# Kernel optimization log

Hardware: AMD Instinct MI355X
Metric: run time of the kernel (lower is better)

Reference implementation:

```python
import jax, jax.numpy as jnp
import numpy as np

NUM_USER = 50000
NUM_ITEM = 30000
N = NUM_USER + NUM_ITEM
E = 300000
DIM = 64
NUM_ROUTING = 3
EPS = 1e-12
SLOPE = 0.01  # torch leaky_relu default negative slope


def l2norm(x):
    return x / jnp.sqrt(jnp.sum(x * x, axis=-1, keepdims=True) + EPS)


def gat_conv(x, src, dst):
    # GRCN GATConv: alpha_e = softmax_{e: dst(e)=i}( <x_i, x_j> ), out_i = sum alpha_e * x_j
    xi = x[dst]                      # [E', D]
    xj = x[src]                      # [E', D]
    a = jnp.sum(xi * xj, axis=-1)    # [E']
    m = jax.ops.segment_max(a, dst, num_segments=N)
    m = jnp.where(jnp.isfinite(m), m, 0.0)  # nodes with no incoming edges
    ea = jnp.exp(a - m[dst])
    s = jax.ops.segment_sum(ea, dst, num_segments=N)
    alpha = ea / (s[dst] + EPS)
    out = jax.ops.segment_sum(xj * alpha[:, None], dst, num_segments=N)
    return out, alpha


def sage_conv(x, src, dst, w_e, W, b):
    # GRCN SAGEConv(aggr='add') with edge weights: out = (sum_j w_e * x_j) @ W + b
    agg = jax.ops.segment_sum(x[src] * w_e, dst, num_segments=N)
    return agg @ W + b


def cgcn(feat, Wm, bm, pref, edge_u, edge_i, src2, dst2):
    f = jax.nn.leaky_relu(feat @ Wm + bm, SLOPE)   # MLP projection, [num_item, D]
    pref = l2norm(pref)
    f = l2norm(f)
    for _ in range(NUM_ROUTING):
        x = jnp.concatenate([pref, f], axis=0)     # [N, D]
        xh, _ = gat_conv(x, edge_i, edge_u)        # items -> users only
        pref = l2norm(pref + xh[:NUM_USER])
    x = jnp.concatenate([pref, f], axis=0)
    xh, alpha = gat_conv(x, src2, dst2)            # doubled (bidirectional) edges
    xh = jax.nn.leaky_relu(xh, SLOPE)
    return x + xh, alpha[:, None]                  # [N, D], [2E, 1]


def egcn(id_emb, src2, dst2, w, W1, b1, W2, b2):
    x = l2norm(id_emb)
    x1 = jax.nn.leaky_relu(sage_conv(x, src2, dst2, w, W1, b1), SLOPE)
    x2 = jax.nn.leaky_relu(sage_conv(x1, src2, dst2, w, W2, b2), SLOPE)
    return x + x1 + x2


def setup_inputs() -> dict:
    key = jax.random.key(0)
    ks = jax.random.split(key, 16)
    edge_u = jax.random.randint(ks[0], (E,), 0, NUM_USER)
    edge_i = jax.random.randint(ks[1], (E,), NUM_USER, N)  # items offset by NUM_USER
    xav = lambda k, sh: jax.random.normal(k, sh, jnp.float32) * np.float32(np.sqrt(2.0 / (sh[0] + sh[1])))
    return {
        'edge_u': edge_u,
        'edge_i': edge_i,
        'v_feat': jax.random.normal(ks[2], (NUM_ITEM, 2048), jnp.float32),
        'a_feat': jax.random.normal(ks[3], (NUM_ITEM, 128), jnp.float32),
        'pref_v': xav(ks[4], (NUM_USER, DIM)),
        'pref_a': xav(ks[5], (NUM_USER, DIM)),
        'Wv': xav(ks[6], (2048, DIM)),
        'bv': jnp.zeros((DIM,), jnp.float32),
        'Wa': xav(ks[7], (128, DIM)),
        'ba': jnp.zeros((DIM,), jnp.float32),
        'id_emb': xav(ks[8], (N, DIM)),
        'W1': xav(ks[9], (DIM, DIM)),
        'b1': jnp.zeros((DIM,), jnp.float32),
        'W2': xav(ks[10], (DIM, DIM)),
        'b2': jnp.zeros((DIM,), jnp.float32),
        'conf': xav(ks[11], (N, 2)),
    }


def reference(edge_u, edge_i, v_feat, a_feat, pref_v, pref_a, Wv, bv, Wa, ba,
              id_emb, W1, b1, W2, b2, conf):
    # doubled edge list: edge_index cat edge_index[[1,0]], target = row 0
    src2 = jnp.concatenate([edge_i, edge_u])       # [2E]
    dst2 = jnp.concatenate([edge_u, edge_i])       # [2E]

    v_rep, w_v = cgcn(v_feat, Wv, bv, pref_v, edge_u, edge_i, src2, dst2)
    a_rep, w_a = cgcn(a_feat, Wa, ba, pref_a, edge_u, edge_i, src2, dst2)

    weight = jnp.concatenate([w_v, w_a], axis=1)   # [2E, 2]
    # 'confid' mode: confidence = cat(conf[edge[0]], conf[edge[1]]) == conf[dst2]
    confidence = conf[dst2]                        # [2E, 2]
    weight = jnp.max(weight * confidence, axis=1, keepdims=True)  # [2E, 1]
    weight = jax.nn.relu(weight)                   # pruning

    id_rep = egcn(id_emb, src2, dst2, weight, W1, b1, W2, b2)
    # fusion_mode == 'concat'
    return jnp.concatenate([id_rep, v_rep, a_rep], axis=1)  # [N, 3*DIM]
```

## Files before the change

### kernel.cpp

```cpp
#include <hip/hip_runtime.h>
#include <hip/hip_bf16.h>

#define NU 50000
#define NI 30000
#define NN 80000
#define EE 300000
#define E2 600000
#define EPSF 1e-12f
#define SLOPE_ 0.01f
#define NB_SCAN ((NN + 255)/256)

__device__ __forceinline__ float leaky(float v){ return v>0.f? v : SLOPE_*v; }

__device__ __forceinline__ float qred16(float v){
  v += __shfl_xor(v, 1, 16);
  v += __shfl_xor(v, 2, 16);
  v += __shfl_xor(v, 4, 16);
  v += __shfl_xor(v, 8, 16);
  return v;
}
__device__ __forceinline__ float4 qnorm(float4 v){
  float ss = qred16(v.x*v.x + v.y*v.y + v.z*v.z + v.w*v.w);
  float inv = 1.f/sqrtf(ss + EPSF);
  v.x*=inv; v.y*=inv; v.z*=inv; v.w*=inv;
  return v;
}

typedef __attribute__((address_space(3))) unsigned int lds_u32;
typedef const __attribute__((address_space(1))) unsigned int glb_u32;
__device__ __forceinline__ void gld16(const float* g, float* l){
  __builtin_amdgcn_global_load_lds((glb_u32*)g, (lds_u32*)l, 16, 0, 0);
}

__global__ void k_hist(const int* __restrict__ eu, const int* __restrict__ ei, int* __restrict__ cnt){
  int e = blockIdx.x*blockDim.x + threadIdx.x;
  if(e<EE){ atomicAdd(&cnt[eu[e]],1); atomicAdd(&cnt[ei[e]],1); }
}

__global__ void k_scanA(const int* __restrict__ cnt, int* __restrict__ loc, int* __restrict__ bsum){
  __shared__ int sm[256];
  int t = threadIdx.x;
  int i = blockIdx.x*256 + t;
  int v = (i<NN) ? cnt[i] : 0;
  sm[t] = v; __syncthreads();
  #pragma unroll
  for(int off=1; off<256; off<<=1){
    int u = (t>=off) ? sm[t-off] : 0;
    __syncthreads();
    sm[t] += u;
    __syncthreads();
  }
  if(i<NN) loc[i] = sm[t] - v;
  if(t==255) bsum[blockIdx.x] = sm[255];
}

__global__ void k_scanB(int* __restrict__ bsum, int* __restrict__ boff){
  __shared__ int sm[512];
  int t = threadIdx.x;
  int v = (t<NB_SCAN) ? bsum[t] : 0;
  sm[t] = v; __syncthreads();
  #pragma unroll
  for(int off=1; off<512; off<<=1){
    int u = (t>=off) ? sm[t-off] : 0;
    __syncthreads();
    sm[t] += u;
    __syncthreads();
  }
  if(t<NB_SCAN) boff[t] = sm[t] - v;
}

__global__ void k_scanC(const int* __restrict__ loc, const int* __restrict__ boff,
                        int* __restrict__ ptr, int* __restrict__ cur){
  int i = blockIdx.x*256 + threadIdx.x;
  if(i<NN){
    int p = loc[i] + boff[blockIdx.x];
    ptr[i] = p; cur[i] = p;
  }
  if(i==0) ptr[NN] = E2;
}

__global__ void k_scatter(const int* __restrict__ eu, const int* __restrict__ ei,
                          int* __restrict__ cur, int* __restrict__ colA, int* __restrict__ dstA){
  int e = blockIdx.x*blockDim.x + threadIdx.x;
  if(e<EE){
    int u = eu[e], it = ei[e];
    int s1 = atomicAdd(&cur[u],1);  colA[s1]=it; dstA[s1]=u;
    int s2 = atomicAdd(&cur[it],1); colA[s2]=u;  dstA[s2]=it;
  }
}

__global__ void k_l2n4(const float* __restrict__ in, float* __restrict__ out, int rows){
  int idx = blockIdx.x*blockDim.x + threadIdx.x;
  int g = idx>>4, c = idx&15;
  if(g>=rows) return;
  float4 v = *(const float4*)(in + (size_t)g*64 + 4*c);
  *(float4*)(out + (size_t)g*64 + 4*c) = qnorm(v);
}

template<int K, int KS>
__global__ __launch_bounds__(256,4) void k_pg(const float* __restrict__ feat,
    const float* __restrict__ W, float* __restrict__ part, int rows){
  __shared__ float As[64*64];
  __shared__ float Ws[64*64];
  const int KSL = K/KS;
  const int STEPS = KSL/64;
  int t = threadIdx.x;
  int w = t>>6, lane = t&63;
  int c = t&15, rg = t>>4;
  int rowb = blockIdx.x*64;
  int k0 = blockIdx.y*KSL;
  float4 acc[4];
  #pragma unroll
  for(int r=0;r<4;r++) acc[r] = make_float4(0.f,0.f,0.f,0.f);

  for(int s=0; s<STEPS; ++s){
    if(s) __syncthreads();
    int kk = k0 + s*64;
    #pragma unroll
    for(int i=0;i<4;i++){
      int q = w*4 + i;
      int trow = q*4 + (lane>>4);
      int grow = rowb + trow; if(grow > rows-1) grow = rows-1;
      int seg = (lane&15) ^ (q&3);
      gld16(feat + (size_t)grow*K + kk + seg*4, As + q*256);
    }
    #pragma unroll
    for(int i=0;i<4;i++){
      int q = w*4 + i;
      gld16(W + (size_t)(kk + q*4)*64 + lane*4, Ws + q*256);
    }
    __syncthreads();
    #pragma unroll 4
    for(int k4=0;k4<16;k4++){
      float4 wv[4], a4[4];
      #pragma unroll
      for(int j=0;j<4;j++) wv[j] = *(const float4*)&Ws[(k4*4+j)*64 + c*4];
      int sw = (k4 ^ (rg&3))*4;
      #pragma unroll
      for(int r=0;r<4;r++) a4[r] = *(const float4*)&As[(rg*4+r)*64 + sw];
      #pragma unroll
      for(int r=0;r<4;r++){
        acc[r].x += a4[r].x*wv[0].x + a4[r].y*wv[1].x + a4[r].z*wv[2].x + a4[r].w*wv[3].x;
        acc[r].y += a4[r].x*wv[0].y + a4[r].y*wv[1].y + a4[r].z*wv[2].y + a4[r].w*wv[3].y;
        acc[r].z += a4[r].x*wv[0].z + a4[r].y*wv[1].z + a4[r].z*wv[2].z + a4[r].w*wv[3].z;
        acc[r].w += a4[r].x*wv[0].w + a4[r].y*wv[1].w + a4[r].z*wv[2].w + a4[r].w*wv[3].w;
      }
    }
  }
  float* pb = part + (size_t)blockIdx.y*rows*64;
  #pragma unroll
  for(int r=0;r<4;r++){
    int row = rowb + rg*4 + r;
    if(row < rows) *(float4*)(pb + (size_t)row*64 + c*4) = acc[r];
  }
}

template<int KS>
__global__ void k_projfin(const float* __restrict__ part, const float* __restrict__ bias,
    float* __restrict__ xout, int rows){
  int idx = blockIdx.x*blockDim.x + threadIdx.x;
  int g = idx>>4, c = idx&15;
  if(g>=rows) return;
  float4 o = make_float4(0.f,0.f,0.f,0.f);
  #pragma unroll
  for(int s=0;s<KS;s++){
    float4 p = *(const float4*)(part + ((size_t)s*rows + g)*64 + 4*c);
    o.x += p.x; o.y += p.y; o.z += p.z; o.w += p.w;
  }
  float4 bb = *(const float4*)(bias + 4*c);
  o.x = leaky(o.x + bb.x); o.y = leaky(o.y + bb.y);
  o.z = leaky(o.z + bb.z); o.w = leaky(o.w + bb.w);
  *(float4*)(xout + (size_t)g*128 + 4*c) = qnorm(o);
}

__global__ void k_route3(const float* __restrict__ pv, const float* __restrict__ pa,
    float* __restrict__ xc, const int* __restrict__ ptr, const int* __restrict__ col){
  int g = blockIdx.x*(blockDim.x>>4) + (threadIdx.x>>4);
  int c = threadIdx.x & 15;
  if(g >= NU) return;
  float4 uv = qnorm(*(const float4*)(pv + (size_t)g*64 + 4*c));
  float4 ua = qnorm(*(const float4*)(pa + (size_t)g*64 + 4*c));
  int e0 = ptr[g], e1 = ptr[g+1];
  #pragma unroll 1
  for(int it=0; it<3; ++it){
    float sv = 0.f, sa = 0.f;
    float4 cv = make_float4(0.f,0.f,0.f,0.f);
    float4 ca = make_float4(0.f,0.f,0.f,0.f);
    for(int e=e0; e<e1; e++){
      int src = col[e];
      float4 jv = *(const float4*)(xc + (size_t)src*128 + 4*c);
      float4 ja = *(const float4*)(xc + (size_t)src*128 + 64 + 4*c);
      float dv = qred16(uv.x*jv.x + uv.y*jv.y + uv.z*jv.z + uv.w*jv.w);
      float da = qred16(ua.x*ja.x + ua.y*ja.y + ua.z*ja.z + ua.w*ja.w);
      float ev = __expf(dv), ea = __expf(da);
      sv += ev; sa += ea;
      cv.x += ev*jv.x; cv.y += ev*jv.y; cv.z += ev*jv.z; cv.w += ev*jv.w;
      ca.x += ea*ja.x; ca.y += ea*ja.y; ca.z += ea*ja.z; ca.w += ea*ja.w;
    }
    float iv = 1.f/(sv + EPSF), ia = 1.f/(sa + EPSF);
    uv = qnorm(make_float4(uv.x + cv.x*iv, uv.y + cv.y*iv, uv.z + cv.z*iv, uv.w + cv.w*iv));
    ua = qnorm(make_float4(ua.x + ca.x*ia, ua.y + ca.y*ia, ua.z + ca.z*ia, ua.w + ca.w*ia));
  }
  *(float4*)(xc + (size_t)g*128 + 4*c) = uv;
  *(float4*)(xc + (size_t)g*128 + 64 + 4*c) = ua;
}

__global__ void k_fgat(const float* __restrict__ xc,
    float* __restrict__ av, float* __restrict__ aa,
    float* __restrict__ sv, float* __restrict__ sa,
    const int* __restrict__ ptr, const int* __restrict__ col,
    float* __restrict__ out){
  int g = blockIdx.x*(blockDim.x>>4) + (threadIdx.x>>4);
  int c = threadIdx.x & 15;
  if(g >= NN) return;
  float4 iv = *(const float4*)(xc + (size_t)g*128 + 4*c);
  float4 ia = *(const float4*)(xc + (size_t)g*128 + 64 + 4*c);
  int e0 = ptr[g], e1 = ptr[g+1];
  float smv = 0.f, sma = 0.f;
  float4 cv = make_float4(0.f,0.f,0.f,0.f);
  float4 ca = make_float4(0.f,0.f,0.f,0.f);
  for(int e=e0; e<e1; e++){
    int src = col[e];
    float4 jv = *(const float4*)(xc + (size_t)src*128 + 4*c);
    float4 ja = *(const float4*)(xc + (size_t)src*128 + 64 + 4*c);
    float dv = qred16(iv.x*jv.x + iv.y*jv.y + iv.z*jv.z + iv.w*jv.w);
    float da = qred16(ia.x*ja.x + ia.y*ja.y + ia.z*ja.z + ia.w*ja.w);
    float ev = __expf(dv), ea = __expf(da);
    if(c==0){ av[e] = ev; aa[e] = ea; }
    smv += ev; sma += ea;
    cv.x += ev*jv.x; cv.y += ev*jv.y; cv.z += ev*jv.z; cv.w += ev*jv.w;
    ca.x += ea*ja.x; ca.y += ea*ja.y; ca.z += ea*ja.z; ca.w += ea*ja.w;
  }
  float invv = 1.f/(smv + EPSF), inva = 1.f/(sma + EPSF);
  if(c==0){ sv[g] = invv; sa[g] = inva; }
  float4 ov = make_float4(iv.x + leaky(cv.x*invv), iv.y + leaky(cv.y*invv),
                          iv.z + leaky(cv.z*invv), iv.w + leaky(cv.w*invv));
  float4 oa = make_float4(ia.x + leaky(ca.x*inva), ia.y + leaky(ca.y*inva),
                          ia.z + leaky(ca.z*inva), ia.w + leaky(ca.w*inva));
  *(float4*)(out + (size_t)g*192 + 64  + 4*c) = ov;
  *(float4*)(out + (size_t)g*192 + 128 + 4*c) = oa;
}

__global__ void k_weight(const float* __restrict__ av, const float* __restrict__ aa,
    const float* __restrict__ sv, const float* __restrict__ sa,
    const int* __restrict__ dstA, const float* __restrict__ conf, float* __restrict__ w){
  int e = blockIdx.x*blockDim.x + threadIdx.x;
  if(e >= E2) return;
  int d = dstA[e];
  float wv = av[e]*sv[d]*conf[2*d+0];
  float wa = aa[e]*sa[d]*conf[2*d+1];
  float m = fmaxf(wv, wa);
  w[e] = (m > 0.f) ? m : 0.f;
}

template<int EPI>
__global__ __launch_bounds__(256) void k_aggmm(const float* __restrict__ xin,
    const float* __restrict__ wb, const int* __restrict__ ptr, const int* __restrict__ col,
    const float* __restrict__ Wm, const float* __restrict__ bm,
    const float* __restrict__ a0, const float* __restrict__ a1,
    float* __restrict__ outp){
  __shared__ float Wl[64*64];
  __shared__ float rowbuf[16*68];
  int t = threadIdx.x;
  #pragma unroll
  for(int i=0;i<4;i++)
    *(float4*)&Wl[i*1024 + t*4] = *(const float4*)&Wm[i*1024 + t*4];
  int grp = t>>4, c = t&15;
  int g = blockIdx.x*16 + grp;
  bool ok = g < NN;
  int e0 = ok ? ptr[g] : 0, e1 = ok ? ptr[g+1] : 0;
  float4 acc = make_float4(0.f,0.f,0.f,0.f);
  for(int e=e0; e<e1; e++){
    float we = wb[e];
    float4 xs = *(const float4*)(xin + (size_t)col[e]*64 + 4*c);
    acc.x += we*xs.x; acc.y += we*xs.y; acc.z += we*xs.z; acc.w += we*xs.w;
  }
  __syncthreads();
  *(float4*)&rowbuf[grp*68 + c*4] = acc;
  float4 o = make_float4(0.f,0.f,0.f,0.f);
  #pragma unroll 4
  for(int k4=0;k4<16;k4++){
    float4 a4 = *(const float4*)&rowbuf[grp*68 + k4*4];
    float4 w0 = *(const float4*)&Wl[(k4*4+0)*64 + c*4];
    float4 w1 = *(const float4*)&Wl[(k4*4+1)*64 + c*4];
    float4 w2 = *(const float4*)&Wl[(k4*4+2)*64 + c*4];
    float4 w3 = *(const float4*)&Wl[(k4*4+3)*64 + c*4];
    o.x += a4.x*w0.x + a4.y*w1.x + a4.z*w2.x + a4.w*w3.x;
    o.y += a4.x*w0.y + a4.y*w1.y + a4.z*w2.y + a4.w*w3.y;
    o.z += a4.x*w0.z + a4.y*w1.z + a4.z*w2.z + a4.w*w3.z;
    o.w += a4.x*w0.w + a4.y*w1.w + a4.z*w2.w + a4.w*w3.w;
  }
  if(!ok) return;
  float4 bb = *(const float4*)(bm + 4*c);
  o.x = leaky(o.x + bb.x); o.y = leaky(o.y + bb.y);
  o.z = leaky(o.z + bb.z); o.w = leaky(o.w + bb.w);
  if(EPI==0){
    *(float4*)(outp + (size_t)g*64 + 4*c) = o;
  }else{
    float4 v0 = *(const float4*)(a0 + (size_t)g*64 + 4*c);
    float4 v1 = *(const float4*)(a1 + (size_t)g*64 + 4*c);
    o.x += v0.x + v1.x; o.y += v0.y + v1.y;
    o.z += v0.z + v1.z; o.w += v0.w + v1.w;
    *(float4*)(outp + (size_t)g*192 + 4*c) = o;
  }
}

extern "C" void kernel_launch(void* const* d_in, const int* in_sizes, int n_in,
                              void* d_out, int out_size, void* d_ws, size_t ws_size,
                              hipStream_t stream){
  const int*   edge_u = (const int*)  d_in[0];
  const int*   edge_i = (const int*)  d_in[1];
  const float* v_feat = (const float*)d_in[2];
  const float* a_feat = (const float*)d_in[3];
  const float* pref_v = (const float*)d_in[4];
  const float* pref_a = (const float*)d_in[5];
  const float* Wv     = (const float*)d_in[6];
  const float* bv     = (const float*)d_in[7];
  const float* Wa     = (const float*)d_in[8];
  const float* ba     = (const float*)d_in[9];
  const float* id_emb = (const float*)d_in[10];
  const float* W1     = (const float*)d_in[11];
  const float* b1     = (const float*)d_in[12];
  const float* W2     = (const float*)d_in[13];
  const float* b2     = (const float*)d_in[14];
  const float* conf   = (const float*)d_in[15];
  float* out = (float*)d_out;

  char* p = (char*)d_ws;
  auto alloc = [&](size_t bytes)->void*{
    void* q = p; p += (bytes + 255) & ~(size_t)255; return q;
  };
  int*   cnt  = (int*)  alloc((size_t)NN*4);
  int*   loc  = (int*)  alloc((size_t)NN*4);
  int*   bsum = (int*)  alloc((size_t)NB_SCAN*4);
  int*   boff = (int*)  alloc((size_t)NB_SCAN*4);
  int*   ptr  = (int*)  alloc((size_t)(NN+1)*4);
  int*   cur  = (int*)  alloc((size_t)NN*4);
  int*   colA = (int*)  alloc((size_t)E2*4);
  int*   dstA = (int*)  alloc((size_t)E2*4);
  float* xc   = (float*)alloc((size_t)NN*128*4);
  float* x0   = (float*)alloc((size_t)NN*64*4);
  float* x1   = (float*)alloc((size_t)NN*64*4);
  float* av   = (float*)alloc((size_t)E2*4);
  float* aa   = (float*)alloc((size_t)E2*4);
  float* sv   = (float*)alloc((size_t)NN*4);
  float* sa   = (float*)alloc((size_t)NN*4);
  float* wb   = (float*)alloc((size_t)E2*4);
  float* part = x0;

  hipMemsetAsync(cnt, 0, (size_t)NN*4, stream);
  k_hist<<<(EE+255)/256, 256, 0, stream>>>(edge_u, edge_i, cnt);
  k_scanA<<<NB_SCAN, 256, 0, stream>>>(cnt, loc, bsum);
  k_scanB<<<1, 512, 0, stream>>>(bsum, boff);
  k_scanC<<<NB_SCAN, 256, 0, stream>>>(loc, boff, ptr, cur);
  k_scatter<<<(EE+255)/256, 256, 0, stream>>>(edge_u, edge_i, cur, colA, dstA);

  k_pg<2048,4><<<dim3((NI+63)/64, 4), 256, 0, stream>>>(v_feat, Wv, part, NI);
  k_projfin<4><<<(NI*16+255)/256, 256, 0, stream>>>(part, bv, xc + (size_t)NU*128, NI);
  k_pg<128,2><<<dim3((NI+63)/64, 2), 256, 0, stream>>>(a_feat, Wa, part, NI);
  k_projfin<2><<<(NI*16+255)/256, 256, 0, stream>>>(part, ba, xc + (size_t)NU*128 + 64, NI);

  k_l2n4<<<(NN*16+255)/256, 256, 0, stream>>>(id_emb, x0, NN);

  k_route3<<<(NU+15)/16, 256, 0, stream>>>(pref_v, pref_a, xc, ptr, colA);

  k_fgat<<<(NN+15)/16, 256, 0, stream>>>(xc, av, aa, sv, sa, ptr, colA, out);

  k_weight<<<(E2+255)/256, 256, 0, stream>>>(av, aa, sv, sa, dstA, conf, wb);

  k_aggmm<0><<<(NN+15)/16, 256, 0, stream>>>(x0, wb, ptr, colA, W1, b1, nullptr, nullptr, x1);
  k_aggmm<1><<<(NN+15)/16, 256, 0, stream>>>(x1, wb, ptr, colA, W2, b2, x0, x1, out);
}
```

Before: 751.3 us.

## Fuse edge-weight kernel into aggmm, widen gather groups, enlarge projection tile

Several changes land together. The k_weight kernel and the dstA array are removed, and the pruned edge weights are now computed inside the first aggregation kernel using per-destination sums and confidences. The route and final GAT kernels now use 32-lane groups covering both modalities in one row, with neighbour loops unrolled by two for more memory-level parallelism. The visual projection GEMM moves to a 128-row tile to increase reuse of the weight tile. Together these cut a launch and the dstA traffic and improve gather throughput, at the cost of higher register use in the larger GEMM tile.

```diff
diff --git a/kernel.cpp b/kernel.cpp
--- a/kernel.cpp
+++ b/kernel.cpp
@@ -25,6 +25,9 @@
   v.x*=inv; v.y*=inv; v.z*=inv; v.w*=inv;
   return v;
 }
+__device__ __forceinline__ float dot4(float4 a, float4 b){
+  return a.x*b.x + a.y*b.y + a.z*b.z + a.w*b.w;
+}
 
 typedef __attribute__((address_space(3))) unsigned int lds_u32;
 typedef const __attribute__((address_space(1))) unsigned int glb_u32;
@@ -80,12 +83,12 @@
 }
 
 __global__ void k_scatter(const int* __restrict__ eu, const int* __restrict__ ei,
-                          int* __restrict__ cur, int* __restrict__ colA, int* __restrict__ dstA){
+                          int* __restrict__ cur, int* __restrict__ colA){
   int e = blockIdx.x*blockDim.x + threadIdx.x;
   if(e<EE){
     int u = eu[e], it = ei[e];
-    int s1 = atomicAdd(&cur[u],1);  colA[s1]=it; dstA[s1]=u;
-    int s2 = atomicAdd(&cur[it],1); colA[s2]=u;  dstA[s2]=it;
+    int s1 = atomicAdd(&cur[u],1);  colA[s1]=it;
+    int s2 = atomicAdd(&cur[it],1); colA[s2]=u;
   }
 }
 
@@ -95,6 +98,63 @@
   if(g>=rows) return;
   float4 v = *(const float4*)(in + (size_t)g*64 + 4*c);
   *(float4*)(out + (size_t)g*64 + 4*c) = qnorm(v);
+}
+
+template<int K, int KS>
+__global__ __launch_bounds__(256,4) void k_pg128(const float* __restrict__ feat,
+    const float* __restrict__ W, float* __restrict__ part, int rows){
+  __shared__ float As[128*64];
+  __shared__ float Ws[64*64];
+  const int KSL = K/KS;
+  const int STEPS = KSL/64;
+  int t = threadIdx.x;
+  int w = t>>6, lane = t&63;
+  int c = t&15, rg = t>>4;
+  int rowb = blockIdx.x*128;
+  int k0 = blockIdx.y*KSL;
+  float4 acc[8];
+  #pragma unroll
+  for(int r=0;r<8;r++) acc[r] = make_float4(0.f,0.f,0.f,0.f);
+
+  for(int s=0; s<STEPS; ++s){
+    if(s) __syncthreads();
+    int kk = k0 + s*64;
+    #pragma unroll
+    for(int i=0;i<8;i++){
+      int q = w*8 + i;
+      int grow = rowb + q*4 + (lane>>4); if(grow > rows-1) grow = rows-1;
+      int seg = (lane&15) ^ (q&3);
+      gld16(feat + (size_t)grow*K + kk + seg*4, As + q*256);
+    }
+    #pragma unroll
+    for(int i=0;i<4;i++){
+      int q = w*4 + i;
+      gld16(W + (size_t)(kk + q*4)*64 + lane*4, Ws + q*256);
+    }
+    __syncthreads();
+    #pragma unroll 2
+    for(int k4=0;k4<16;k4++){
+      float4 wv[4];
+      #pragma unroll
+      for(int j=0;j<4;j++) wv[j] = *(const float4*)&Ws[(k4*4+j)*64 + c*4];
+      #pragma unroll
+      for(int r=0;r<8;r++){
+        int row = rg*8 + r;
+        int sw = (k4 ^ ((row>>2)&3))*4;
+        float4 a4 = *(const float4*)&As[row*64 + sw];
+        acc[r].x += a4.x*wv[0].x + a4.y*wv[1].x + a4.z*wv[2].x + a4.w*wv[3].x;
+        acc[r].y += a4.x*wv[0].y + a4.y*wv[1].y + a4.z*wv[2].y + a4.w*wv[3].y;
+        acc[r].z += a4.x*wv[0].z + a4.y*wv[1].z + a4.z*wv[2].z + a4.w*wv[3].z;
+        acc[r].w += a4.x*wv[0].w + a4.y*wv[1].w + a4.z*wv[2].w + a4.w*wv[3].w;
+      }
+    }
+  }
+  float* pb = part + (size_t)blockIdx.y*rows*64;
+  #pragma unroll
+  for(int r=0;r<8;r++){
+    int row = rowb + rg*8 + r;
+    if(row < rows) *(float4*)(pb + (size_t)row*64 + c*4) = acc[r];
+  }
 }
 
 template<int K, int KS>
@@ -119,8 +179,7 @@
     #pragma unroll
     for(int i=0;i<4;i++){
       int q = w*4 + i;
-      int trow = q*4 + (lane>>4);
-      int grow = rowb + trow; if(grow > rows-1) grow = rows-1;
+      int grow = rowb + q*4 + (lane>>4); if(grow > rows-1) grow = rows-1;
       int seg = (lane&15) ^ (q&3);
       gld16(feat + (size_t)grow*K + kk + seg*4, As + q*256);
     }
@@ -175,34 +234,40 @@
 
 __global__ void k_route3(const float* __restrict__ pv, const float* __restrict__ pa,
     float* __restrict__ xc, const int* __restrict__ ptr, const int* __restrict__ col){
-  int g = blockIdx.x*(blockDim.x>>4) + (threadIdx.x>>4);
-  int c = threadIdx.x & 15;
+  int g = blockIdx.x*8 + (threadIdx.x>>5);
+  int c = threadIdx.x & 31;
   if(g >= NU) return;
-  float4 uv = qnorm(*(const float4*)(pv + (size_t)g*64 + 4*c));
-  float4 ua = qnorm(*(const float4*)(pa + (size_t)g*64 + 4*c));
+  float4 u = (c<16) ? *(const float4*)(pv + (size_t)g*64 + 4*c)
+                    : *(const float4*)(pa + (size_t)g*64 + 4*(c-16));
+  u = qnorm(u);
   int e0 = ptr[g], e1 = ptr[g+1];
   #pragma unroll 1
   for(int it=0; it<3; ++it){
-    float sv = 0.f, sa = 0.f;
-    float4 cv = make_float4(0.f,0.f,0.f,0.f);
-    float4 ca = make_float4(0.f,0.f,0.f,0.f);
-    for(int e=e0; e<e1; e++){
-      int src = col[e];
-      float4 jv = *(const float4*)(xc + (size_t)src*128 + 4*c);
-      float4 ja = *(const float4*)(xc + (size_t)src*128 + 64 + 4*c);
-      float dv = qred16(uv.x*jv.x + uv.y*jv.y + uv.z*jv.z + uv.w*jv.w);
-      float da = qred16(ua.x*ja.x + ua.y*ja.y + ua.z*ja.z + ua.w*ja.w);
-      float ev = __expf(dv), ea = __expf(da);
-      sv += ev; sa += ea;
-      cv.x += ev*jv.x; cv.y += ev*jv.y; cv.z += ev*jv.z; cv.w += ev*jv.w;
-      ca.x += ea*ja.x; ca.y += ea*ja.y; ca.z += ea*ja.z; ca.w += ea*ja.w;
-    }
-    float iv = 1.f/(sv + EPSF), ia = 1.f/(sa + EPSF);
-    uv = qnorm(make_float4(uv.x + cv.x*iv, uv.y + cv.y*iv, uv.z + cv.z*iv, uv.w + cv.w*iv));
-    ua = qnorm(make_float4(ua.x + ca.x*ia, ua.y + ca.y*ia, ua.z + ca.z*ia, ua.w + ca.w*ia));
-  }
-  *(float4*)(xc + (size_t)g*128 + 4*c) = uv;
-  *(float4*)(xc + (size_t)g*128 + 64 + 4*c) = ua;
+    float s = 0.f;
+    float4 acc = make_float4(0.f,0.f,0.f,0.f);
+    int e = e0;
+    for(; e+1<e1; e+=2){
+      int s0 = col[e], s1 = col[e+1];
+      float4 j0 = *(const float4*)(xc + (size_t)s0*128 + 4*c);
+      float4 j1 = *(const float4*)(xc + (size_t)s1*128 + 4*c);
+      float d0 = qred16(dot4(u,j0));
+      float d1 = qred16(dot4(u,j1));
+      float w0 = __expf(d0), w1 = __expf(d1);
+      s += w0 + w1;
+      acc.x += w0*j0.x + w1*j1.x; acc.y += w0*j0.y + w1*j1.y;
+      acc.z += w0*j0.z + w1*j1.z; acc.w += w0*j0.w + w1*j1.w;
+    }
+    if(e<e1){
+      float4 j0 = *(const float4*)(xc + (size_t)col[e]*128 + 4*c);
+      float w0 = __expf(qred16(dot4(u,j0)));
+      s += w0;
+      acc.x += w0*j0.x; acc.y += w0*j0.y; acc.z += w0*j0.z; acc.w += w0*j0.w;
+    }
+    float inv = 1.f/(s + EPSF);
+    u = qnorm(make_float4(u.x + acc.x*inv, u.y + acc.y*inv,
+                          u.z + acc.z*inv, u.w + acc.w*inv));
+  }
+  *(float4*)(xc + (size_t)g*128 + 4*c) = u;
 }
 
 __global__ void k_fgat(const float* __restrict__ xc,
@@ -210,52 +275,49 @@
     float* __restrict__ sv, float* __restrict__ sa,
     const int* __restrict__ ptr, const int* __restrict__ col,
     float* __restrict__ out){
-  int g = blockIdx.x*(blockDim.x>>4) + (threadIdx.x>>4);
-  int c = threadIdx.x & 15;
+  int g = blockIdx.x*8 + (threadIdx.x>>5);
+  int c = threadIdx.x & 31;
   if(g >= NN) return;
-  float4 iv = *(const float4*)(xc + (size_t)g*128 + 4*c);
-  float4 ia = *(const float4*)(xc + (size_t)g*128 + 64 + 4*c);
+  float4 xi = *(const float4*)(xc + (size_t)g*128 + 4*c);
   int e0 = ptr[g], e1 = ptr[g+1];
-  float smv = 0.f, sma = 0.f;
-  float4 cv = make_float4(0.f,0.f,0.f,0.f);
-  float4 ca = make_float4(0.f,0.f,0.f,0.f);
-  for(int e=e0; e<e1; e++){
-    int src = col[e];
-    float4 jv = *(const float4*)(xc + (size_t)src*128 + 4*c);
-    float4 ja = *(const float4*)(xc + (size_t)src*128 + 64 + 4*c);
-    float dv = qred16(iv.x*jv.x + iv.y*jv.y + iv.z*jv.z + iv.w*jv.w);
-    float da = qred16(ia.x*ja.x + ia.y*ja.y + ia.z*ja.z + ia.w*ja.w);
-    float ev = __expf(dv), ea = __expf(da);
-    if(c==0){ av[e] = ev; aa[e] = ea; }
-    smv += ev; sma += ea;
-    cv.x += ev*jv.x; cv.y += ev*jv.y; cv.z += ev*jv.z; cv.w += ev*jv.w;
-    ca.x += ea*ja.x; ca.y += ea*ja.y; ca.z += ea*ja.z; ca.w += ea*ja.w;
-  }
-  float invv = 1.f/(smv + EPSF), inva = 1.f/(sma + EPSF);
-  if(c==0){ sv[g] = invv; sa[g] = inva; }
-  float4 ov = make_float4(iv.x + leaky(cv.x*invv), iv.y + leaky(cv.y*invv),
-                          iv.z + leaky(cv.z*invv), iv.w + leaky(cv.w*invv));
-  float4 oa = make_float4(ia.x + leaky(ca.x*inva), ia.y + leaky(ca.y*inva),
-                          ia.z + leaky(ca.z*inva), ia.w + leaky(ca.w*inva));
-  *(float4*)(out + (size_t)g*192 + 64  + 4*c) = ov;
-  *(float4*)(out + (size_t)g*192 + 128 + 4*c) = oa;
-}
-
-__global__ void k_weight(const float* __restrict__ av, const float* __restrict__ aa,
-    const float* __restrict__ sv, const float* __restrict__ sa,
-    const int* __restrict__ dstA, const float* __restrict__ conf, float* __restrict__ w){
-  int e = blockIdx.x*blockDim.x + threadIdx.x;
-  if(e >= E2) return;
-  int d = dstA[e];
-  float wv = av[e]*sv[d]*conf[2*d+0];
-  float wa = aa[e]*sa[d]*conf[2*d+1];
-  float m = fmaxf(wv, wa);
-  w[e] = (m > 0.f) ? m : 0.f;
+  float s = 0.f;
+  float4 acc = make_float4(0.f,0.f,0.f,0.f);
+  int e = e0;
+  for(; e+1<e1; e+=2){
+    int s0 = col[e], s1 = col[e+1];
+    float4 j0 = *(const float4*)(xc + (size_t)s0*128 + 4*c);
+    float4 j1 = *(const float4*)(xc + (size_t)s1*128 + 4*c);
+    float d0 = qred16(dot4(xi,j0));
+    float d1 = qred16(dot4(xi,j1));
+    float w0 = __expf(d0), w1 = __expf(d1);
+    if(c==0){  av[e] = w0; av[e+1] = w1; }
+    if(c==16){ aa[e] = w0; aa[e+1] = w1; }
+    s += w0 + w1;
+    acc.x += w0*j0.x + w1*j1.x; acc.y += w0*j0.y + w1*j1.y;
+    acc.z += w0*j0.z + w1*j1.z; acc.w += w0*j0.w + w1*j1.w;
+  }
+  if(e<e1){
+    float4 j0 = *(const float4*)(xc + (size_t)col[e]*128 + 4*c);
+    float w0 = __expf(qred16(dot4(xi,j0)));
+    if(c==0)  av[e] = w0;
+    if(c==16) aa[e] = w0;
+    s += w0;
+    acc.x += w0*j0.x; acc.y += w0*j0.y; acc.z += w0*j0.z; acc.w += w0*j0.w;
+  }
+  float inv = 1.f/(s + EPSF);
+  if(c==0)  sv[g] = inv;
+  if(c==16) sa[g] = inv;
+  float4 o = make_float4(xi.x + leaky(acc.x*inv), xi.y + leaky(acc.y*inv),
+                         xi.z + leaky(acc.z*inv), xi.w + leaky(acc.w*inv));
+  *(float4*)(out + (size_t)g*192 + 64 + 4*c) = o;
 }
 
 template<int EPI>
 __global__ __launch_bounds__(256) void k_aggmm(const float* __restrict__ xin,
-    const float* __restrict__ wb, const int* __restrict__ ptr, const int* __restrict__ col,
+    const float* __restrict__ av, const float* __restrict__ aa,
+    const float* __restrict__ sv, const float* __restrict__ sa,
+    const float* __restrict__ conf, float* __restrict__ wb,
+    const int* __restrict__ ptr, const int* __restrict__ col,
     const float* __restrict__ Wm, const float* __restrict__ bm,
     const float* __restrict__ a0, const float* __restrict__ a1,
     float* __restrict__ outp){
@@ -268,12 +330,34 @@
   int grp = t>>4, c = t&15;
   int g = blockIdx.x*16 + grp;
   bool ok = g < NN;
+  int gg = ok ? g : 0;
   int e0 = ok ? ptr[g] : 0, e1 = ok ? ptr[g+1] : 0;
+  float c0=0.f, c1=0.f, isv=0.f, isa=0.f;
+  if(EPI==0){ c0 = conf[2*gg]; c1 = conf[2*gg+1]; isv = sv[gg]; isa = sa[gg]; }
   float4 acc = make_float4(0.f,0.f,0.f,0.f);
-  for(int e=e0; e<e1; e++){
-    float we = wb[e];
-    float4 xs = *(const float4*)(xin + (size_t)col[e]*64 + 4*c);
-    acc.x += we*xs.x; acc.y += we*xs.y; acc.z += we*xs.z; acc.w += we*xs.w;
+  int e = e0;
+  for(; e+1<e1; e+=2){
+    float w0, w1;
+    if(EPI==0){
+      w0 = fmaxf(fmaxf(av[e]*isv*c0,   aa[e]*isa*c1),   0.f);
+      w1 = fmaxf(fmaxf(av[e+1]*isv*c0, aa[e+1]*isa*c1), 0.f);
+      if(c==0){ wb[e] = w0; wb[e+1] = w1; }
+    }else{
+      w0 = wb[e]; w1 = wb[e+1];
+    }
+    float4 x0v = *(const float4*)(xin + (size_t)col[e]*64 + 4*c);
+    float4 x1v = *(const float4*)(xin + (size_t)col[e+1]*64 + 4*c);
+    acc.x += w0*x0v.x + w1*x1v.x; acc.y += w0*x0v.y + w1*x1v.y;
+    acc.z += w0*x0v.z + w1*x1v.z; acc.w += w0*x0v.w + w1*x1v.w;
+  }
+  if(e<e1){
+    float w0;
+    if(EPI==0){
+      w0 = fmaxf(fmaxf(av[e]*isv*c0, aa[e]*isa*c1), 0.f);
+      if(c==0) wb[e] = w0;
+    }else w0 = wb[e];
+    float4 x0v = *(const float4*)(xin + (size_t)col[e]*64 + 4*c);
+    acc.x += w0*x0v.x; acc.y += w0*x0v.y; acc.z += w0*x0v.z; acc.w += w0*x0v.w;
   }
   __syncthreads();
   *(float4*)&rowbuf[grp*68 + c*4] = acc;
@@ -337,7 +421,6 @@
   int*   ptr  = (int*)  alloc((size_t)(NN+1)*4);
   int*   cur  = (int*)  alloc((size_t)NN*4);
   int*   colA = (int*)  alloc((size_t)E2*4);
-  int*   dstA = (int*)  alloc((size_t)E2*4);
   float* xc   = (float*)alloc((size_t)NN*128*4);
   float* x0   = (float*)alloc((size_t)NN*64*4);
   float* x1   = (float*)alloc((size_t)NN*64*4);
@@ -353,21 +436,21 @@
   k_scanA<<<NB_SCAN, 256, 0, stream>>>(cnt, loc, bsum);
   k_scanB<<<1, 512, 0, stream>>>(bsum, boff);
   k_scanC<<<NB_SCAN, 256, 0, stream>>>(loc, boff, ptr, cur);
-  k_scatter<<<(EE+255)/256, 256, 0, stream>>>(edge_u, edge_i, cur, colA, dstA);
-
-  k_pg<2048,4><<<dim3((NI+63)/64, 4), 256, 0, stream>>>(v_feat, Wv, part, NI);
+  k_scatter<<<(EE+255)/256, 256, 0, stream>>>(edge_u, edge_i, cur, colA);
+
+  k_pg128<2048,4><<<dim3((NI+127)/128, 4), 256, 0, stream>>>(v_feat, Wv, part, NI);
   k_projfin<4><<<(NI*16+255)/256, 256, 0, stream>>>(part, bv, xc + (size_t)NU*128, NI);
   k_pg<128,2><<<dim3((NI+63)/64, 2), 256, 0, stream>>>(a_feat, Wa, part, NI);
   k_projfin<2><<<(NI*16+255)/256, 256, 0, stream>>>(part, ba, xc + (size_t)NU*128 + 64, NI);
 
   k_l2n4<<<(NN*16+255)/256, 256, 0, stream>>>(id_emb, x0, NN);
 
-  k_route3<<<(NU+15)/16, 256, 0, stream>>>(pref_v, pref_a, xc, ptr, colA);
-
-  k_fgat<<<(NN+15)/16, 256, 0, stream>>>(xc, av, aa, sv, sa, ptr, colA, out);
-
-  k_weight<<<(E2+255)/256, 256, 0, stream>>>(av, aa, sv, sa, dstA, conf, wb);
-
-  k_aggmm<0><<<(NN+15)/16, 256, 0, stream>>>(x0, wb, ptr, colA, W1, b1, nullptr, nullptr, x1);
-  k_aggmm<1><<<(NN+15)/16, 256, 0, stream>>>(x1, wb, ptr, colA, W2, b2, x0, x1, out);
-}
+  k_route3<<<(NU+7)/8, 256, 0, stream>>>(pref_v, pref_a, xc, ptr, colA);
+
+  k_fgat<<<(NN+7)/8, 256, 0, stream>>>(xc, av, aa, sv, sa, ptr, colA, out);
+
+  k_aggmm<0><<<(NN+15)/16, 256, 0, stream>>>(x0, av, aa, sv, sa, conf, wb,
+                                             ptr, colA, W1, b1, nullptr, nullptr, x1);
+  k_aggmm<1><<<(NN+15)/16, 256, 0, stream>>>(x1, av, aa, sv, sa, conf, wb,
+                                             ptr, colA, W2, b2, x0, x1, out);
+}
```

Result: no change. 736.8 us (-1.9%).
